# Kernel tuning notes

Measured on AMD Instinct MI355X. Metric: run time of the kernel, lower is better.

The kernel has to match this reference:

```python
import jax, jax.numpy as jnp
import numpy as np
from jax import lax

B, D, RANK, HID = 8192, 4096, 16, 24


def setup_inputs() -> dict:
    key = jax.random.key(0)
    ks = jax.random.split(key, 12)
    return {
        "grad": jax.random.normal(ks[0], (B, D), jnp.float32),
        "embed": jax.random.normal(ks[1], (B, D), jnp.float32),
        # LRLinear layer 0 (init='id' -> randn)
        "u0": jax.random.normal(ks[2], (D, RANK), jnp.float32),
        "v0": jax.random.normal(ks[3], (RANK, D), jnp.float32),
        "b0": jnp.zeros((D,), jnp.float32),
        # LRLinear layer 1
        "u1": jax.random.normal(ks[4], (D, RANK), jnp.float32),
        "v1": jax.random.normal(ks[5], (RANK, D), jnp.float32),
        "b1": jnp.zeros((D,), jnp.float32),
        # coeff MLP: Linear(D, HID) -> ReLU -> Linear(HID, 1) -> sigmoid
        "w1": jax.random.normal(ks[6], (HID, D), jnp.float32) * 0.02,
        "bw1": jnp.zeros((HID,), jnp.float32),
        "w2": jax.random.normal(ks[7], (1, HID), jnp.float32) * 0.02,
        "bw2": jnp.zeros((1,), jnp.float32),
    }


def _lr_layer(x, u, v, b):
    # (u @ (v @ x.T)).T + b, clamped at 0  ==  relu(x @ v.T @ u.T + b)
    return jnp.maximum((x @ v.T) @ u.T + b, 0.0)


def reference(grad, embed, u0, v0, b0, u1, v1, b1, w1, bw1, w2, bw2):
    grad_ = grad.reshape(-1, grad.shape[-1]).astype(jnp.float32)  # [B, D]
    k = grad_.shape[0]

    # Welford running mean / S over the batch, fused into one parallel
    # reduction (mathematically identical to the sequential update_counter).
    mean = jnp.mean(grad_, axis=0)                       # grad_mean [D]
    s = jnp.sum((grad_ - mean) ** 2, axis=0)             # grad_s    [D]
    std = jnp.sqrt(s / (k - 1))                          # grad_std  [D]
    mean = lax.stop_gradient(mean)
    std = lax.stop_gradient(std)

    # norm=True path
    x0 = (grad_ - mean) / (std + 1e-7)                   # [B, D]

    # IDMLP: low-rank relu chain
    x = _lr_layer(x0, u0, v0, b0)
    x = _lr_layer(x, u1, v1, b1)

    # choice == 0: per-row L2 renormalization to x0's row norms
    xn = jnp.sqrt(jnp.sum(x ** 2, axis=1)) + 1e-8        # [B]
    x0n = jnp.sqrt(jnp.sum(x0 ** 2, axis=1)) + 1e-8      # [B]
    x = x / xn[:, None] * x0n[:, None]

    # coeff MLP on embed
    h = jnp.maximum(embed @ w1.T + bw1, 0.0)             # [B, HID]
    coeff = jax.nn.sigmoid(h @ w2.T + bw2)               # [B, 1]

    out = (1.0 - coeff) * x + coeff * x0                 # [B, D]
    return out, coeff
```

## Files before the change

kernel.cpp:

```cpp
#include <hip/hip_runtime.h>
#include <math.h>

#define BN 8192
#define DD 4096
#define RK 16
#define HIDN 24
#define NCHUNK 32

#define OFF_T0T  0
#define OFF_T1T  (OFF_T0T + RK*BN)
#define OFF_HT   (OFF_T1T + RK*BN)
#define OFF_XN2  (OFF_HT + 32*BN)
#define OFF_X0N2 (OFF_XN2 + BN)
#define ZCOUNT   (OFF_X0N2 + BN)
#define OFF_V1T  (ZCOUNT)
#define OFF_MEAN (OFF_V1T + DD*RK)
#define OFF_INV  (OFF_MEAN + DD)
#define OFF_COEF (OFF_INV + DD)

typedef __attribute__((ext_vector_type(8))) __bf16 bf16x8;
typedef __attribute__((ext_vector_type(4))) float f32x4;

__device__ inline void split8(const float* __restrict__ p, bf16x8& hi, bf16x8& lo) {
    float4 a = *(const float4*)p;
    float4 b = *(const float4*)(p + 4);
    float v[8] = {a.x, a.y, a.z, a.w, b.x, b.y, b.z, b.w};
#pragma unroll
    for (int j = 0; j < 8; ++j) {
        __bf16 h = (__bf16)v[j];
        hi[j] = h;
        lo[j] = (__bf16)(v[j] - (float)h);
    }
}

__global__ __launch_bounds__(256) void kT(const float* __restrict__ v1,
                                          float* __restrict__ v1T) {
    int d = blockIdx.x * 256 + threadIdx.x;
    float v[16];
#pragma unroll
    for (int s = 0; s < 16; ++s) v[s] = v1[(size_t)s * DD + d];
#pragma unroll
    for (int s = 0; s < 4; ++s)
        *(float4*)(v1T + (size_t)d * 16 + s * 4) =
            make_float4(v[4 * s], v[4 * s + 1], v[4 * s + 2], v[4 * s + 3]);
}

__global__ __launch_bounds__(256) void k1a(const float* __restrict__ g,
                                           float* __restrict__ ps,
                                           float* __restrict__ pq) {
    int ct = blockIdx.x & 15, rc = blockIdx.x >> 4;
    int col = ct * 256 + threadIdx.x;
    size_t base = (size_t)rc * 256 * DD + col;
    float s1 = 0.f, s2 = 0.f;
#pragma unroll 4
    for (int i = 0; i < 256; ++i) {
        float v = g[base + (size_t)i * DD];
        s1 += v;
        s2 = fmaf(v, v, s2);
    }
    ps[rc * DD + col] = s1;
    pq[rc * DD + col] = s2;
}

__global__ __launch_bounds__(256) void k1b(const float* __restrict__ ps,
                                           const float* __restrict__ pq,
                                           float* __restrict__ meanw,
                                           float* __restrict__ invw) {
    int d = blockIdx.x * 256 + threadIdx.x;
    float s1 = 0.f, s2 = 0.f;
#pragma unroll
    for (int i = 0; i < NCHUNK; ++i) {
        s1 += ps[i * DD + d];
        s2 += pq[i * DD + d];
    }
    float mean = s1 / (float)BN;
    float var = (s2 - s1 * s1 / (float)BN) / (float)(BN - 1);
    var = fmaxf(var, 0.f);
    meanw[d] = mean;
    invw[d] = 1.f / (sqrtf(var) + 1e-7f);
}

__global__ __launch_bounds__(256) void k2m(const float* __restrict__ grad,
                                           const float* __restrict__ meanw,
                                           const float* __restrict__ invw,
                                           const float* __restrict__ v0,
                                           float* __restrict__ T0T,
                                           float* __restrict__ X0N2) {
    __shared__ float red[4][512];
    int tid = threadIdx.x;
    int wv = tid >> 6, l = tid & 63;
    int lr = l & 15, lk = l >> 4;
    int m0 = (blockIdx.x >> 2) * 32;
    int kbase = (blockIdx.x & 3) * 1024 + wv * 256;
    const float* g0 = grad + (size_t)(m0 + lr) * DD + kbase + lk * 8;
    const float* vp = v0 + (size_t)lr * DD + kbase + lk * 8;
    const float* mp = meanw + kbase + lk * 8;
    const float* ip = invw + kbase + lk * 8;
    f32x4 acc[2] = {};
    float xs[2] = {0.f, 0.f};
#pragma unroll 2
    for (int ks = 0; ks < 8; ++ks) {
        int k0 = ks * 32;
        bf16x8 vhi, vlo;
        split8(vp + k0, vhi, vlo);
        float4 ma = *(const float4*)(mp + k0);
        float4 mb = *(const float4*)(mp + k0 + 4);
        float4 ia = *(const float4*)(ip + k0);
        float4 ib = *(const float4*)(ip + k0 + 4);
        float mv[8] = {ma.x, ma.y, ma.z, ma.w, mb.x, mb.y, mb.z, mb.w};
        float iv[8] = {ia.x, ia.y, ia.z, ia.w, ib.x, ib.y, ib.z, ib.w};
#pragma unroll
        for (int mt = 0; mt < 2; ++mt) {
            float4 ga = *(const float4*)(g0 + (size_t)(mt * 16) * DD + k0);
            float4 gb = *(const float4*)(g0 + (size_t)(mt * 16) * DD + k0 + 4);
            float gv[8] = {ga.x, ga.y, ga.z, ga.w, gb.x, gb.y, gb.z, gb.w};
            bf16x8 xhi, xlo;
            float ss = 0.f;
#pragma unroll
            for (int j = 0; j < 8; ++j) {
                float x = (gv[j] - mv[j]) * iv[j];
                ss = fmaf(x, x, ss);
                __bf16 h = (__bf16)x;
                xhi[j] = h;
                xlo[j] = (__bf16)(x - (float)h);
            }
            xs[mt] += ss;
            acc[mt] = __builtin_amdgcn_mfma_f32_16x16x32_bf16(vhi, xhi, acc[mt], 0, 0, 0);
            acc[mt] = __builtin_amdgcn_mfma_f32_16x16x32_bf16(vhi, xlo, acc[mt], 0, 0, 0);
            acc[mt] = __builtin_amdgcn_mfma_f32_16x16x32_bf16(vlo, xhi, acc[mt], 0, 0, 0);
        }
    }
    float s0 = xs[0], s1 = xs[1];
    s0 += __shfl_xor(s0, 16); s0 += __shfl_xor(s0, 32);
    s1 += __shfl_xor(s1, 16); s1 += __shfl_xor(s1, 32);
    if (l < 16) {
        atomicAdd(&X0N2[m0 + lr], s0);
        atomicAdd(&X0N2[m0 + 16 + lr], s1);
    }
#pragma unroll
    for (int mt = 0; mt < 2; ++mt)
#pragma unroll
        for (int r = 0; r < 4; ++r)
            red[wv][mt * 256 + (lk * 4 + r) * 16 + lr] = acc[mt][r];
    __syncthreads();
    int o = tid * 2;
    int mt = (tid >> 7) & 1, nr = (tid >> 3) & 15;
#pragma unroll
    for (int j = 0; j < 2; ++j) {
        float s = red[0][o + j] + red[1][o + j] + red[2][o + j] + red[3][o + j];
        atomicAdd(&T0T[(size_t)nr * BN + m0 + mt * 16 + (o & 15) + j], s);
    }
}

__global__ __launch_bounds__(256) void k3(const float* __restrict__ T0T,
                                          const float* __restrict__ u0,
                                          const float* __restrict__ b0,
                                          const float* __restrict__ v1T,
                                          float* __restrict__ T1T) {
    int b = (blockIdx.x >> 5) * 256 + threadIdx.x;
    int d0 = (blockIdx.x & 31) * 128;
    float t0[16];
#pragma unroll
    for (int r = 0; r < 16; ++r) t0[r] = T0T[(size_t)r * BN + b];
    float acc[16];
#pragma unroll
    for (int s = 0; s < 16; ++s) acc[s] = 0.f;
#pragma unroll 2
    for (int d = d0; d < d0 + 128; ++d) {
        const float* ur = u0 + (size_t)d * RK;
        float x1 = b0[d];
#pragma unroll
        for (int r = 0; r < 16; ++r) x1 = fmaf(ur[r], t0[r], x1);
        x1 = fmaxf(x1, 0.f);
        const float* vr = v1T + (size_t)d * RK;
#pragma unroll
        for (int s = 0; s < 16; ++s) acc[s] = fmaf(vr[s], x1, acc[s]);
    }
#pragma unroll
    for (int s = 0; s < 16; ++s)
        atomicAdd(&T1T[(size_t)s * BN + b], acc[s]);
}

__global__ __launch_bounds__(256) void k4(const float* __restrict__ T1T,
                                          const float* __restrict__ u1,
                                          const float* __restrict__ b1,
                                          float* __restrict__ XN2) {
    int b = (blockIdx.x >> 5) * 256 + threadIdx.x;
    int d0 = (blockIdx.x & 31) * 128;
    float t1[16];
#pragma unroll
    for (int r = 0; r < 16; ++r) t1[r] = T1T[(size_t)r * BN + b];
    float acc = 0.f;
#pragma unroll 2
    for (int d = d0; d < d0 + 128; ++d) {
        const float* ur = u1 + (size_t)d * RK;
        float x = b1[d];
#pragma unroll
        for (int r = 0; r < 16; ++r) x = fmaf(ur[r], t1[r], x);
        x = fmaxf(x, 0.f);
        acc = fmaf(x, x, acc);
    }
    atomicAdd(&XN2[b], acc);
}

__global__ __launch_bounds__(256) void k5m(const float* __restrict__ embed,
                                           const float* __restrict__ w1,
                                           float* __restrict__ HT) {
    __shared__ float red[4][1024];
    int tid = threadIdx.x;
    int wv = tid >> 6, l = tid & 63;
    int lr = l & 15, lk = l >> 4;
    int m0 = (blockIdx.x >> 2) * 32;
    int kbase = (blockIdx.x & 3) * 1024 + wv * 256;
    int wr1 = (lr + 16 > 23) ? 23 : lr + 16;
    const float* e0 = embed + (size_t)(m0 + lr) * DD + kbase + lk * 8;
    const float* w0a = w1 + (size_t)lr * DD + kbase + lk * 8;
    const float* w0b = w1 + (size_t)wr1 * DD + kbase + lk * 8;
    f32x4 acc[2][2] = {};
#pragma unroll 2
    for (int ks = 0; ks < 8; ++ks) {
        int k0 = ks * 32;
        bf16x8 whi0, wlo0, whi1, wlo1;
        split8(w0a + k0, whi0, wlo0);
        split8(w0b + k0, whi1, wlo1);
#pragma unroll
        for (int mt = 0; mt < 2; ++mt) {
            bf16x8 ehi, elo;
            split8(e0 + (size_t)(mt * 16) * DD + k0, ehi, elo);
            acc[mt][0] = __builtin_amdgcn_mfma_f32_16x16x32_bf16(whi0, ehi, acc[mt][0], 0, 0, 0);
            acc[mt][1] = __builtin_amdgcn_mfma_f32_16x16x32_bf16(whi1, ehi, acc[mt][1], 0, 0, 0);
            acc[mt][0] = __builtin_amdgcn_mfma_f32_16x16x32_bf16(whi0, elo, acc[mt][0], 0, 0, 0);
            acc[mt][1] = __builtin_amdgcn_mfma_f32_16x16x32_bf16(whi1, elo, acc[mt][1], 0, 0, 0);
            acc[mt][0] = __builtin_amdgcn_mfma_f32_16x16x32_bf16(wlo0, ehi, acc[mt][0], 0, 0, 0);
            acc[mt][1] = __builtin_amdgcn_mfma_f32_16x16x32_bf16(wlo1, ehi, acc[mt][1], 0, 0, 0);
        }
    }
#pragma unroll
    for (int mt = 0; mt < 2; ++mt)
#pragma unroll
        for (int nt = 0; nt < 2; ++nt)
#pragma unroll
            for (int r = 0; r < 4; ++r)
                red[wv][(mt * 2 + nt) * 256 + (lk * 4 + r) * 16 + lr] = acc[mt][nt][r];
    __syncthreads();
    int o = tid * 4;
    int mt = (tid >> 7) & 1, nt = (tid >> 6) & 1, nr = (tid >> 2) & 15;
#pragma unroll
    for (int j = 0; j < 4; ++j) {
        float s = red[0][o + j] + red[1][o + j] + red[2][o + j] + red[3][o + j];
        atomicAdd(&HT[(size_t)(nt * 16 + nr) * BN + m0 + mt * 16 + (o & 15) + j], s);
    }
}

__global__ __launch_bounds__(256) void k5b(const float* __restrict__ HT,
                                           const float* __restrict__ bw1,
                                           const float* __restrict__ w2,
                                           const float* __restrict__ bw2,
                                           float* __restrict__ COEF,
                                           float* __restrict__ out) {
    int b = blockIdx.x * 256 + threadIdx.x;
    float z = bw2[0];
#pragma unroll
    for (int j = 0; j < HIDN; ++j) {
        float h = fmaxf(HT[(size_t)j * BN + b] + bw1[j], 0.f);
        z = fmaf(w2[j], h, z);
    }
    float cf = 1.f / (1.f + expf(-z));
    COEF[b] = cf;
    out[(size_t)BN * DD + b] = cf;
}

__device__ inline float dotu(const float4* ur, const float* t, float b) {
    float a = b;
#pragma unroll
    for (int rr = 0; rr < 4; ++rr) {
        a = fmaf(ur[rr].x, t[4 * rr + 0], a);
        a = fmaf(ur[rr].y, t[4 * rr + 1], a);
        a = fmaf(ur[rr].z, t[4 * rr + 2], a);
        a = fmaf(ur[rr].w, t[4 * rr + 3], a);
    }
    return a;
}

__global__ __launch_bounds__(256) void k6(const float* __restrict__ grad,
                                          const float* __restrict__ meanw,
                                          const float* __restrict__ invw,
                                          const float* __restrict__ T1T,
                                          const float* __restrict__ u1,
                                          const float* __restrict__ b1,
                                          const float* __restrict__ XN2,
                                          const float* __restrict__ X0N2,
                                          const float* __restrict__ COEF,
                                          float* __restrict__ out) {
    int tid = threadIdx.x;
    int rt = blockIdx.x >> 2, ct = blockIdx.x & 3;
    int row0 = rt * 16, col0 = ct * 1024;
    int c = col0 + tid * 4;
    float4 u[4][4];
#pragma unroll
    for (int cc = 0; cc < 4; ++cc)
#pragma unroll
        for (int rr = 0; rr < 4; ++rr)
            u[cc][rr] = *(const float4*)(u1 + (size_t)(c + cc) * RK + rr * 4);
    float4 bv = *(const float4*)(b1 + c);
    float4 mv = *(const float4*)(meanw + c);
    float4 iv = *(const float4*)(invw + c);

    for (int row = 0; row < 16; ++row) {
        int b = row0 + row;
        float t[16];
#pragma unroll
        for (int r = 0; r < 16; ++r) t[r] = T1T[(size_t)r * BN + b];
        float4 g = *(const float4*)(grad + (size_t)b * DD + c);
        float4 x0;
        x0.x = (g.x - mv.x) * iv.x;
        x0.y = (g.y - mv.y) * iv.y;
        x0.z = (g.z - mv.z) * iv.z;
        x0.w = (g.w - mv.w) * iv.w;
        float4 x2;
        x2.x = fmaxf(dotu(u[0], t, bv.x), 0.f);
        x2.y = fmaxf(dotu(u[1], t, bv.y), 0.f);
        x2.z = fmaxf(dotu(u[2], t, bv.z), 0.f);
        x2.w = fmaxf(dotu(u[3], t, bv.w), 0.f);
        float cf = COEF[b];
        float x0n = sqrtf(X0N2[b]) + 1e-8f;
        float xn = sqrtf(XN2[b]) + 1e-8f;
        float s1 = (1.f - cf) * x0n / xn;
        float4 o;
        o.x = fmaf(s1, x2.x, cf * x0.x);
        o.y = fmaf(s1, x2.y, cf * x0.y);
        o.z = fmaf(s1, x2.z, cf * x0.z);
        o.w = fmaf(s1, x2.w, cf * x0.w);
        *(float4*)(out + (size_t)b * DD + c) = o;
    }
}

extern "C" void kernel_launch(void* const* d_in, const int* in_sizes, int n_in,
                              void* d_out, int out_size, void* d_ws, size_t ws_size,
                              hipStream_t stream) {
    const float* grad = (const float*)d_in[0];
    const float* embed = (const float*)d_in[1];
    const float* u0 = (const float*)d_in[2];
    const float* v0 = (const float*)d_in[3];
    const float* b0 = (const float*)d_in[4];
    const float* u1 = (const float*)d_in[5];
    const float* v1 = (const float*)d_in[6];
    const float* b1 = (const float*)d_in[7];
    const float* w1 = (const float*)d_in[8];
    const float* bw1 = (const float*)d_in[9];
    const float* w2 = (const float*)d_in[10];
    const float* bw2 = (const float*)d_in[11];
    float* out = (float*)d_out;
    float* ws = (float*)d_ws;

    hipMemsetAsync(ws, 0, (size_t)ZCOUNT * sizeof(float), stream);

    kT<<<16, 256, 0, stream>>>(v1, ws + OFF_V1T);
    k5m<<<1024, 256, 0, stream>>>(embed, w1, ws + OFF_HT);
    k1a<<<512, 256, 0, stream>>>(grad, ws + OFF_T0T, ws + OFF_T1T);
    k1b<<<16, 256, 0, stream>>>(ws + OFF_T0T, ws + OFF_T1T, ws + OFF_MEAN, ws + OFF_INV);
    hipMemsetAsync(ws + OFF_T0T, 0, (size_t)(2 * RK * BN) * sizeof(float), stream);
    k2m<<<1024, 256, 0, stream>>>(grad, ws + OFF_MEAN, ws + OFF_INV, v0,
                                  ws + OFF_T0T, ws + OFF_X0N2);
    k3<<<1024, 256, 0, stream>>>(ws + OFF_T0T, u0, b0, ws + OFF_V1T, ws + OFF_T1T);
    k4<<<1024, 256, 0, stream>>>(ws + OFF_T1T, u1, b1, ws + OFF_XN2);
    k5b<<<32, 256, 0, stream>>>(ws + OFF_HT, bw1, w2, bw2, ws + OFF_COEF, out);
    k6<<<2048, 256, 0, stream>>>(grad, ws + OFF_MEAN, ws + OFF_INV, ws + OFF_T1T,
                                 u1, b1, ws + OFF_XN2, ws + OFF_X0N2,
                                 ws + OFF_COEF, out);
}
```

Measured before the change: 540.6 us.

## Fuse row-norm computation into final kernel and drop k4 pass

Removes the separate k4 kernel, which recomputed the second low-rank layer only to get row norms. The final kernel now runs one 1024-thread block per 16 rows covering the full width, so it can compute both x and x0 row norms in-block with shuffle and shared-memory reductions. k1a is vectorized with float4 loads over more chunks. k2m and k5m drop to 16-row tiles with twice the blocks, and the memset between stats and k2m is removed by giving the partial sums their own workspace. The cost is two __syncthreads per row in the final kernel and less reuse of the weight splits in the MFMA kernels.

```diff
diff --git a/kernel.cpp b/kernel.cpp
--- a/kernel.cpp
+++ b/kernel.cpp
@@ -5,15 +5,15 @@
 #define DD 4096
 #define RK 16
 #define HIDN 24
-#define NCHUNK 32
+#define NCHUNK 128
 
 #define OFF_T0T  0
 #define OFF_T1T  (OFF_T0T + RK*BN)
 #define OFF_HT   (OFF_T1T + RK*BN)
-#define OFF_XN2  (OFF_HT + 32*BN)
-#define OFF_X0N2 (OFF_XN2 + BN)
-#define ZCOUNT   (OFF_X0N2 + BN)
-#define OFF_V1T  (ZCOUNT)
+#define ZCOUNT   (OFF_HT + 32*BN)
+#define OFF_PS   (ZCOUNT)
+#define OFF_PQ   (OFF_PS + NCHUNK*DD)
+#define OFF_V1T  (OFF_PQ + NCHUNK*DD)
 #define OFF_MEAN (OFF_V1T + DD*RK)
 #define OFF_INV  (OFF_MEAN + DD)
 #define OFF_COEF (OFF_INV + DD)
@@ -48,18 +48,22 @@
 __global__ __launch_bounds__(256) void k1a(const float* __restrict__ g,
                                            float* __restrict__ ps,
                                            float* __restrict__ pq) {
-    int ct = blockIdx.x & 15, rc = blockIdx.x >> 4;
-    int col = ct * 256 + threadIdx.x;
-    size_t base = (size_t)rc * 256 * DD + col;
-    float s1 = 0.f, s2 = 0.f;
-#pragma unroll 4
-    for (int i = 0; i < 256; ++i) {
-        float v = g[base + (size_t)i * DD];
-        s1 += v;
-        s2 = fmaf(v, v, s2);
-    }
-    ps[rc * DD + col] = s1;
-    pq[rc * DD + col] = s2;
+    int ct = blockIdx.x & 3, rc = blockIdx.x >> 2;
+    int col = ct * 1024 + threadIdx.x * 4;
+    size_t base = (size_t)rc * 64 * DD + col;
+    float4 s1 = make_float4(0.f, 0.f, 0.f, 0.f);
+    float4 s2 = make_float4(0.f, 0.f, 0.f, 0.f);
+#pragma unroll 8
+    for (int i = 0; i < 64; ++i) {
+        float4 v = *(const float4*)(g + base + (size_t)i * DD);
+        s1.x += v.x; s1.y += v.y; s1.z += v.z; s1.w += v.w;
+        s2.x = fmaf(v.x, v.x, s2.x);
+        s2.y = fmaf(v.y, v.y, s2.y);
+        s2.z = fmaf(v.z, v.z, s2.z);
+        s2.w = fmaf(v.w, v.w, s2.w);
+    }
+    *(float4*)(ps + (size_t)rc * DD + col) = s1;
+    *(float4*)(pq + (size_t)rc * DD + col) = s2;
 }
 
 __global__ __launch_bounds__(256) void k1b(const float* __restrict__ ps,
@@ -68,7 +72,7 @@
                                            float* __restrict__ invw) {
     int d = blockIdx.x * 256 + threadIdx.x;
     float s1 = 0.f, s2 = 0.f;
-#pragma unroll
+#pragma unroll 8
     for (int i = 0; i < NCHUNK; ++i) {
         s1 += ps[i * DD + d];
         s2 += pq[i * DD + d];
@@ -84,20 +88,18 @@
                                            const float* __restrict__ meanw,
                                            const float* __restrict__ invw,
                                            const float* __restrict__ v0,
-                                           float* __restrict__ T0T,
-                                           float* __restrict__ X0N2) {
-    __shared__ float red[4][512];
+                                           float* __restrict__ T0T) {
+    __shared__ float red[4][256];
     int tid = threadIdx.x;
     int wv = tid >> 6, l = tid & 63;
     int lr = l & 15, lk = l >> 4;
-    int m0 = (blockIdx.x >> 2) * 32;
+    int m0 = (blockIdx.x >> 2) * 16;
     int kbase = (blockIdx.x & 3) * 1024 + wv * 256;
     const float* g0 = grad + (size_t)(m0 + lr) * DD + kbase + lk * 8;
     const float* vp = v0 + (size_t)lr * DD + kbase + lk * 8;
     const float* mp = meanw + kbase + lk * 8;
     const float* ip = invw + kbase + lk * 8;
-    f32x4 acc[2] = {};
-    float xs[2] = {0.f, 0.f};
+    f32x4 acc = {0.f, 0.f, 0.f, 0.f};
 #pragma unroll 2
     for (int ks = 0; ks < 8; ++ks) {
         int k0 = ks * 32;
@@ -109,47 +111,27 @@
         float4 ib = *(const float4*)(ip + k0 + 4);
         float mv[8] = {ma.x, ma.y, ma.z, ma.w, mb.x, mb.y, mb.z, mb.w};
         float iv[8] = {ia.x, ia.y, ia.z, ia.w, ib.x, ib.y, ib.z, ib.w};
-#pragma unroll
-        for (int mt = 0; mt < 2; ++mt) {
-            float4 ga = *(const float4*)(g0 + (size_t)(mt * 16) * DD + k0);
-            float4 gb = *(const float4*)(g0 + (size_t)(mt * 16) * DD + k0 + 4);
-            float gv[8] = {ga.x, ga.y, ga.z, ga.w, gb.x, gb.y, gb.z, gb.w};
-            bf16x8 xhi, xlo;
-            float ss = 0.f;
-#pragma unroll
-            for (int j = 0; j < 8; ++j) {
-                float x = (gv[j] - mv[j]) * iv[j];
-                ss = fmaf(x, x, ss);
-                __bf16 h = (__bf16)x;
-                xhi[j] = h;
-                xlo[j] = (__bf16)(x - (float)h);
-            }
-            xs[mt] += ss;
-            acc[mt] = __builtin_amdgcn_mfma_f32_16x16x32_bf16(vhi, xhi, acc[mt], 0, 0, 0);
-            acc[mt] = __builtin_amdgcn_mfma_f32_16x16x32_bf16(vhi, xlo, acc[mt], 0, 0, 0);
-            acc[mt] = __builtin_amdgcn_mfma_f32_16x16x32_bf16(vlo, xhi, acc[mt], 0, 0, 0);
+        float4 ga = *(const float4*)(g0 + k0);
+        float4 gb = *(const float4*)(g0 + k0 + 4);
+        float gv[8] = {ga.x, ga.y, ga.z, ga.w, gb.x, gb.y, gb.z, gb.w};
+        bf16x8 xhi, xlo;
+#pragma unroll
+        for (int j = 0; j < 8; ++j) {
+            float x = (gv[j] - mv[j]) * iv[j];
+            __bf16 h = (__bf16)x;
+            xhi[j] = h;
+            xlo[j] = (__bf16)(x - (float)h);
         }
-    }
-    float s0 = xs[0], s1 = xs[1];
-    s0 += __shfl_xor(s0, 16); s0 += __shfl_xor(s0, 32);
-    s1 += __shfl_xor(s1, 16); s1 += __shfl_xor(s1, 32);
-    if (l < 16) {
-        atomicAdd(&X0N2[m0 + lr], s0);
-        atomicAdd(&X0N2[m0 + 16 + lr], s1);
-    }
-#pragma unroll
-    for (int mt = 0; mt < 2; ++mt)
-#pragma unroll
-        for (int r = 0; r < 4; ++r)
-            red[wv][mt * 256 + (lk * 4 + r) * 16 + lr] = acc[mt][r];
+        acc = __builtin_amdgcn_mfma_f32_16x16x32_bf16(vhi, xhi, acc, 0, 0, 0);
+        acc = __builtin_amdgcn_mfma_f32_16x16x32_bf16(vhi, xlo, acc, 0, 0, 0);
+        acc = __builtin_amdgcn_mfma_f32_16x16x32_bf16(vlo, xhi, acc, 0, 0, 0);
+    }
+#pragma unroll
+    for (int r = 0; r < 4; ++r)
+        red[wv][(lk * 4 + r) * 16 + lr] = acc[r];
     __syncthreads();
-    int o = tid * 2;
-    int mt = (tid >> 7) & 1, nr = (tid >> 3) & 15;
-#pragma unroll
-    for (int j = 0; j < 2; ++j) {
-        float s = red[0][o + j] + red[1][o + j] + red[2][o + j] + red[3][o + j];
-        atomicAdd(&T0T[(size_t)nr * BN + m0 + mt * 16 + (o & 15) + j], s);
-    }
+    float s = red[0][tid] + red[1][tid] + red[2][tid] + red[3][tid];
+    atomicAdd(&T0T[(size_t)(tid >> 4) * BN + m0 + (tid & 15)], s);
 }
 
 __global__ __launch_bounds__(256) void k3(const float* __restrict__ T0T,
@@ -181,74 +163,47 @@
         atomicAdd(&T1T[(size_t)s * BN + b], acc[s]);
 }
 
-__global__ __launch_bounds__(256) void k4(const float* __restrict__ T1T,
-                                          const float* __restrict__ u1,
-                                          const float* __restrict__ b1,
-                                          float* __restrict__ XN2) {
-    int b = (blockIdx.x >> 5) * 256 + threadIdx.x;
-    int d0 = (blockIdx.x & 31) * 128;
-    float t1[16];
-#pragma unroll
-    for (int r = 0; r < 16; ++r) t1[r] = T1T[(size_t)r * BN + b];
-    float acc = 0.f;
-#pragma unroll 2
-    for (int d = d0; d < d0 + 128; ++d) {
-        const float* ur = u1 + (size_t)d * RK;
-        float x = b1[d];
-#pragma unroll
-        for (int r = 0; r < 16; ++r) x = fmaf(ur[r], t1[r], x);
-        x = fmaxf(x, 0.f);
-        acc = fmaf(x, x, acc);
-    }
-    atomicAdd(&XN2[b], acc);
-}
-
 __global__ __launch_bounds__(256) void k5m(const float* __restrict__ embed,
                                            const float* __restrict__ w1,
                                            float* __restrict__ HT) {
-    __shared__ float red[4][1024];
+    __shared__ float red[4][512];
     int tid = threadIdx.x;
     int wv = tid >> 6, l = tid & 63;
     int lr = l & 15, lk = l >> 4;
-    int m0 = (blockIdx.x >> 2) * 32;
+    int m0 = (blockIdx.x >> 2) * 16;
     int kbase = (blockIdx.x & 3) * 1024 + wv * 256;
     int wr1 = (lr + 16 > 23) ? 23 : lr + 16;
     const float* e0 = embed + (size_t)(m0 + lr) * DD + kbase + lk * 8;
     const float* w0a = w1 + (size_t)lr * DD + kbase + lk * 8;
     const float* w0b = w1 + (size_t)wr1 * DD + kbase + lk * 8;
-    f32x4 acc[2][2] = {};
+    f32x4 acc0 = {0.f, 0.f, 0.f, 0.f};
+    f32x4 acc1 = {0.f, 0.f, 0.f, 0.f};
 #pragma unroll 2
     for (int ks = 0; ks < 8; ++ks) {
         int k0 = ks * 32;
-        bf16x8 whi0, wlo0, whi1, wlo1;
+        bf16x8 whi0, wlo0, whi1, wlo1, ehi, elo;
         split8(w0a + k0, whi0, wlo0);
         split8(w0b + k0, whi1, wlo1);
-#pragma unroll
-        for (int mt = 0; mt < 2; ++mt) {
-            bf16x8 ehi, elo;
-            split8(e0 + (size_t)(mt * 16) * DD + k0, ehi, elo);
-            acc[mt][0] = __builtin_amdgcn_mfma_f32_16x16x32_bf16(whi0, ehi, acc[mt][0], 0, 0, 0);
-            acc[mt][1] = __builtin_amdgcn_mfma_f32_16x16x32_bf16(whi1, ehi, acc[mt][1], 0, 0, 0);
-            acc[mt][0] = __builtin_amdgcn_mfma_f32_16x16x32_bf16(whi0, elo, acc[mt][0], 0, 0, 0);
-            acc[mt][1] = __builtin_amdgcn_mfma_f32_16x16x32_bf16(whi1, elo, acc[mt][1], 0, 0, 0);
-            acc[mt][0] = __builtin_amdgcn_mfma_f32_16x16x32_bf16(wlo0, ehi, acc[mt][0], 0, 0, 0);
-            acc[mt][1] = __builtin_amdgcn_mfma_f32_16x16x32_bf16(wlo1, ehi, acc[mt][1], 0, 0, 0);
-        }
-    }
-#pragma unroll
-    for (int mt = 0; mt < 2; ++mt)
-#pragma unroll
-        for (int nt = 0; nt < 2; ++nt)
-#pragma unroll
-            for (int r = 0; r < 4; ++r)
-                red[wv][(mt * 2 + nt) * 256 + (lk * 4 + r) * 16 + lr] = acc[mt][nt][r];
+        split8(e0 + k0, ehi, elo);
+        acc0 = __builtin_amdgcn_mfma_f32_16x16x32_bf16(whi0, ehi, acc0, 0, 0, 0);
+        acc1 = __builtin_amdgcn_mfma_f32_16x16x32_bf16(whi1, ehi, acc1, 0, 0, 0);
+        acc0 = __builtin_amdgcn_mfma_f32_16x16x32_bf16(whi0, elo, acc0, 0, 0, 0);
+        acc1 = __builtin_amdgcn_mfma_f32_16x16x32_bf16(whi1, elo, acc1, 0, 0, 0);
+        acc0 = __builtin_amdgcn_mfma_f32_16x16x32_bf16(wlo0, ehi, acc0, 0, 0, 0);
+        acc1 = __builtin_amdgcn_mfma_f32_16x16x32_bf16(wlo1, ehi, acc1, 0, 0, 0);
+    }
+#pragma unroll
+    for (int r = 0; r < 4; ++r) {
+        red[wv][(lk * 4 + r) * 16 + lr] = acc0[r];
+        red[wv][256 + (lk * 4 + r) * 16 + lr] = acc1[r];
+    }
     __syncthreads();
-    int o = tid * 4;
-    int mt = (tid >> 7) & 1, nt = (tid >> 6) & 1, nr = (tid >> 2) & 15;
-#pragma unroll
-    for (int j = 0; j < 4; ++j) {
-        float s = red[0][o + j] + red[1][o + j] + red[2][o + j] + red[3][o + j];
-        atomicAdd(&HT[(size_t)(nt * 16 + nr) * BN + m0 + mt * 16 + (o & 15) + j], s);
+#pragma unroll
+    for (int j = 0; j < 2; ++j) {
+        int idx = tid + j * 256;
+        float s = red[0][idx] + red[1][idx] + red[2][idx] + red[3][idx];
+        int nt = idx >> 8, nr = (idx >> 4) & 15, cc = idx & 15;
+        atomicAdd(&HT[(size_t)(nt * 16 + nr) * BN + m0 + cc], s);
     }
 }
 
@@ -282,20 +237,20 @@
     return a;
 }
 
-__global__ __launch_bounds__(256) void k6(const float* __restrict__ grad,
-                                          const float* __restrict__ meanw,
-                                          const float* __restrict__ invw,
-                                          const float* __restrict__ T1T,
-                                          const float* __restrict__ u1,
-                                          const float* __restrict__ b1,
-                                          const float* __restrict__ XN2,
-                                          const float* __restrict__ X0N2,
-                                          const float* __restrict__ COEF,
-                                          float* __restrict__ out) {
+__global__ __launch_bounds__(1024) void k6f(const float* __restrict__ grad,
+                                            const float* __restrict__ meanw,
+                                            const float* __restrict__ invw,
+                                            const float* __restrict__ T1T,
+                                            const float* __restrict__ u1,
+                                            const float* __restrict__ b1,
+                                            const float* __restrict__ COEF,
+                                            float* __restrict__ out) {
+    __shared__ float redn[2][16];
+    __shared__ float bc[2];
     int tid = threadIdx.x;
-    int rt = blockIdx.x >> 2, ct = blockIdx.x & 3;
-    int row0 = rt * 16, col0 = ct * 1024;
-    int c = col0 + tid * 4;
+    int wv = tid >> 6, l = tid & 63;
+    int row0 = blockIdx.x * 16;
+    int c = tid * 4;
     float4 u[4][4];
 #pragma unroll
     for (int cc = 0; cc < 4; ++cc)
@@ -322,10 +277,35 @@
         x2.y = fmaxf(dotu(u[1], t, bv.y), 0.f);
         x2.z = fmaxf(dotu(u[2], t, bv.z), 0.f);
         x2.w = fmaxf(dotu(u[3], t, bv.w), 0.f);
-        float cf = COEF[b];
-        float x0n = sqrtf(X0N2[b]) + 1e-8f;
-        float xn = sqrtf(XN2[b]) + 1e-8f;
-        float s1 = (1.f - cf) * x0n / xn;
+        float s0 = x0.x * x0.x + x0.y * x0.y + x0.z * x0.z + x0.w * x0.w;
+        float s2 = x2.x * x2.x + x2.y * x2.y + x2.z * x2.z + x2.w * x2.w;
+#pragma unroll
+        for (int off = 1; off < 64; off <<= 1) {
+            s0 += __shfl_xor(s0, off);
+            s2 += __shfl_xor(s2, off);
+        }
+        if (l == 0) {
+            redn[0][wv] = s2;
+            redn[1][wv] = s0;
+        }
+        __syncthreads();
+        if (tid < 16) {
+            float a2 = redn[0][tid], a0 = redn[1][tid];
+#pragma unroll
+            for (int off = 1; off < 16; off <<= 1) {
+                a2 += __shfl_xor(a2, off);
+                a0 += __shfl_xor(a0, off);
+            }
+            if (tid == 0) {
+                float xn = sqrtf(a2) + 1e-8f;
+                float x0n = sqrtf(a0) + 1e-8f;
+                float cf = COEF[b];
+                bc[0] = (1.f - cf) * x0n / xn;
+                bc[1] = cf;
+            }
+        }
+        __syncthreads();
+        float s1 = bc[0], cf = bc[1];
         float4 o;
         o.x = fmaf(s1, x2.x, cf * x0.x);
         o.y = fmaf(s1, x2.y, cf * x0.y);
@@ -356,16 +336,12 @@
     hipMemsetAsync(ws, 0, (size_t)ZCOUNT * sizeof(float), stream);
 
     kT<<<16, 256, 0, stream>>>(v1, ws + OFF_V1T);
-    k5m<<<1024, 256, 0, stream>>>(embed, w1, ws + OFF_HT);
-    k1a<<<512, 256, 0, stream>>>(grad, ws + OFF_T0T, ws + OFF_T1T);
-    k1b<<<16, 256, 0, stream>>>(ws + OFF_T0T, ws + OFF_T1T, ws + OFF_MEAN, ws + OFF_INV);
-    hipMemsetAsync(ws + OFF_T0T, 0, (size_t)(2 * RK * BN) * sizeof(float), stream);
-    k2m<<<1024, 256, 0, stream>>>(grad, ws + OFF_MEAN, ws + OFF_INV, v0,
-                                  ws + OFF_T0T, ws + OFF_X0N2);
+    k5m<<<2048, 256, 0, stream>>>(embed, w1, ws + OFF_HT);
+    k1a<<<512, 256, 0, stream>>>(grad, ws + OFF_PS, ws + OFF_PQ);
+    k1b<<<16, 256, 0, stream>>>(ws + OFF_PS, ws + OFF_PQ, ws + OFF_MEAN, ws + OFF_INV);
+    k2m<<<2048, 256, 0, stream>>>(grad, ws + OFF_MEAN, ws + OFF_INV, v0, ws + OFF_T0T);
     k3<<<1024, 256, 0, stream>>>(ws + OFF_T0T, u0, b0, ws + OFF_V1T, ws + OFF_T1T);
-    k4<<<1024, 256, 0, stream>>>(ws + OFF_T1T, u1, b1, ws + OFF_XN2);
     k5b<<<32, 256, 0, stream>>>(ws + OFF_HT, bw1, w2, bw2, ws + OFF_COEF, out);
-    k6<<<2048, 256, 0, stream>>>(grad, ws + OFF_MEAN, ws + OFF_INV, ws + OFF_T1T,
-                                 u1, b1, ws + OFF_XN2, ws + OFF_X0N2,
-                                 ws + OFF_COEF, out);
-}
+    k6f<<<512, 1024, 0, stream>>>(grad, ws + OFF_MEAN, ws + OFF_INV, ws + OFF_T1T,
+                                  u1, b1, ws + OFF_COEF, out);
+}
```

After: 494.5 us. 8.5% less time.
